# Optimization experiments

Measured on AMD Instinct MI355X. Metric: run time of the kernel, lower is better.

The kernel has to match this reference:

```python
import jax, jax.numpy as jnp
import numpy as np

N = 100000
E = 1600000
IN_FEATS = 512
HIDDEN = 128
NUM_CLASSES = 2


def setup_inputs() -> dict:
    key = jax.random.key(0)
    k1, k2, k3, k4, k5, k6, k7 = jax.random.split(key, 7)
    inputs = jax.random.normal(k1, (N, IN_FEATS), dtype=jnp.float32)
    src = jax.random.randint(k2, (E,), 0, N, dtype=jnp.int64)
    dst = jax.random.randint(k3, (E,), 0, N, dtype=jnp.int64)
    # Glorot-style init like DGL GraphConv
    s1 = (6.0 / (IN_FEATS + HIDDEN)) ** 0.5
    s2 = (6.0 / (HIDDEN + NUM_CLASSES)) ** 0.5
    W1 = jax.random.uniform(k4, (IN_FEATS, HIDDEN), jnp.float32, -s1, s1)
    b1 = jnp.zeros((HIDDEN,), jnp.float32)
    W2 = jax.random.uniform(k5, (HIDDEN, NUM_CLASSES), jnp.float32, -s2, s2)
    b2 = jnp.zeros((NUM_CLASSES,), jnp.float32)
    return {"inputs": inputs, "W1": W1, "b1": b1, "W2": W2, "b2": b2,
            "src": src, "dst": dst}


def _graph_conv(x, W, b, src, dst, norm_src, norm_dst):
    # DGL GraphConv, norm='both': D_dst^{-1/2} A D_src^{-1/2} X W + b
    xw = x @ W                                   # [N, out] dense GEMM first (in >= out)
    m = (xw * norm_src[:, None])[src]            # gather messages [E, out]
    agg = jax.ops.segment_sum(m, dst, num_segments=N)  # scatter-add [N, out]
    return agg * norm_dst[:, None] + b


def reference(inputs, W1, b1, W2, b2, src, dst):
    ones = jnp.ones((src.shape[0],), jnp.float32)
    out_deg = jax.ops.segment_sum(ones, src, num_segments=N)
    in_deg = jax.ops.segment_sum(ones, dst, num_segments=N)
    norm_src = jax.lax.rsqrt(jnp.maximum(out_deg, 1.0))
    norm_dst = jax.lax.rsqrt(jnp.maximum(in_deg, 1.0))

    h = _graph_conv(inputs, W1, b1, src, dst, norm_src, norm_dst)
    h = jax.nn.relu(h)
    # dropout is identity at inference (training=False)
    h = _graph_conv(h, W2, b2, src, dst, norm_src, norm_dst)
    return jax.nn.softmax(h, axis=1)
```

## Files before the change

### kernel.cpp

```cpp
#include <hip/hip_runtime.h>
#include <math.h>

#define N_NODES 100000
#define N_EDGES 1600000
#define IN_F    512
#define HID     128

#define SH      8
#define NPB     256
#define BINS    ((N_NODES + NPB - 1) / NPB)
#define CBLK    256
#define EPB     ((N_EDGES + CBLK - 1) / CBLK)

typedef __attribute__((ext_vector_type(8))) _Float16 half8;
typedef __attribute__((ext_vector_type(2))) _Float16 half2v;
typedef __attribute__((ext_vector_type(4))) float float4v;

__device__ __forceinline__ unsigned int f16_to_e4m3bits(float xs) {
    _Float16 h = (_Float16)xs;
    unsigned short b = __builtin_bit_cast(unsigned short, h);
    unsigned int mag = (unsigned int)(b & 0x7fffu);
    mag = (mag + 0x3fu + ((mag >> 7) & 1u)) >> 7;
    if (mag > 0x7eu) mag = 0x7eu;
    return (((unsigned int)b >> 8) & 0x80u) | mag;
}

__global__ __launch_bounds__(256) void prep_kernel(const float* __restrict__ W1,
                                                   _Float16* __restrict__ W1T,
                                                   int* __restrict__ sdeg) {
    int i = blockIdx.x * 256 + threadIdx.x;
    if (i < IN_F * HID) {
        int k = i >> 7, c = i & 127;
        W1T[(size_t)c * IN_F + k] = (_Float16)W1[i];
    }
    if (i < N_NODES) sdeg[i] = 0;
}

__global__ __launch_bounds__(256) void hist_kernel(const int* __restrict__ src,
                                                   const int* __restrict__ dst,
                                                   int* __restrict__ dbh,
                                                   int* __restrict__ sdeg) {
    __shared__ int hd[BINS];
    const int t = threadIdx.x, blk = blockIdx.x;
    for (int i = t; i < BINS; i += 256) hd[i] = 0;
    __syncthreads();
    const int e0 = blk * EPB, e1 = min(N_EDGES, e0 + EPB);
    for (int e = e0 + t; e < e1; e += 256) {
        atomicAdd(&hd[dst[e] >> SH], 1);
        atomicAdd(&sdeg[src[e]], 1);
    }
    __syncthreads();
    for (int i = t; i < BINS; i += 256)
        dbh[i * CBLK + blk] = hd[i];
}

__global__ __launch_bounds__(256) void binscan_kernel(int* __restrict__ dbh,
                                                      int* __restrict__ dtot) {
    __shared__ int sh[256];
    const int b = blockIdx.x, t = threadIdx.x;
    int* arr = dbh + (size_t)b * CBLK;
    int v = arr[t];
    sh[t] = v; __syncthreads();
#pragma unroll
    for (int d = 1; d < 256; d <<= 1) {
        int u = (t >= d) ? sh[t - d] : 0;
        __syncthreads();
        sh[t] += u;
        __syncthreads();
    }
    arr[t] = sh[t] - v;
    if (t == 255) dtot[b] = sh[255];
}

__global__ __launch_bounds__(512) void binbase_kernel(const int* __restrict__ dtot,
                                                      int* __restrict__ dbase,
                                                      int* __restrict__ offs) {
    __shared__ int sh[512];
    const int t = threadIdx.x;
    int v = (t < BINS) ? dtot[t] : 0;
    sh[t] = v; __syncthreads();
#pragma unroll
    for (int d = 1; d < 512; d <<= 1) {
        int u = (t >= d) ? sh[t - d] : 0;
        __syncthreads();
        sh[t] += u;
        __syncthreads();
    }
    if (t < BINS) dbase[t] = sh[t] - v;
    if (t == BINS - 1) { dbase[BINS] = sh[t]; offs[N_NODES] = sh[t]; }
}

__global__ __launch_bounds__(256) void scatter_bins_kernel(const int* __restrict__ src,
                                                           const int* __restrict__ dst,
                                                           const int* __restrict__ dbh,
                                                           const int* __restrict__ dbase,
                                                           unsigned int* __restrict__ es) {
    __shared__ int dcur[BINS];
    const int t = threadIdx.x, blk = blockIdx.x;
    for (int i = t; i < BINS; i += 256)
        dcur[i] = dbase[i] + dbh[i * CBLK + blk];
    __syncthreads();
    const int e0 = blk * EPB, e1 = min(N_EDGES, e0 + EPB);
    for (int e = e0 + t; e < e1; e += 256) {
        int d = dst[e], s = src[e];
        int p = atomicAdd(&dcur[d >> SH], 1);
        es[p] = ((unsigned int)(d & (NPB - 1)) << 24) | (unsigned int)s;
    }
}

__global__ __launch_bounds__(256) void finalize_kernel(const unsigned int* __restrict__ es,
                                                       const int* __restrict__ sdeg,
                                                       const int* __restrict__ dbase,
                                                       int* __restrict__ csr, int* __restrict__ offs,
                                                       float* __restrict__ norm_dst,
                                                       float* __restrict__ norm_src) {
    __shared__ int cnt[NPB], pos[NPB];
    const int t = threadIdx.x, b = blockIdx.x;
    const int start = dbase[b], end = dbase[b + 1];
    cnt[t] = 0; __syncthreads();
    for (int k = start + t; k < end; k += 256)
        atomicAdd(&cnt[es[k] >> 24], 1);
    __syncthreads();
    const int c = cnt[t];
    pos[t] = c; __syncthreads();
#pragma unroll
    for (int d = 1; d < 256; d <<= 1) {
        int u = (t >= d) ? pos[t - d] : 0;
        __syncthreads();
        pos[t] += u;
        __syncthreads();
    }
    const int excl = pos[t] - c;
    const int node = (b << SH) + t;
    if (node < N_NODES) {
        offs[node] = start + excl;
        norm_dst[node] = rsqrtf(fmaxf((float)c, 1.0f));
        norm_src[node] = rsqrtf(fmaxf((float)sdeg[node], 1.0f));
    }
    cnt[t] = start + excl;
    __syncthreads();
    for (int k = start + t; k < end; k += 256) {
        unsigned int v = es[k];
        int p = atomicAdd(&cnt[v >> 24], 1);
        csr[p] = (int)(v & 0x00FFFFFFu);
    }
}

__global__ __launch_bounds__(256) void gemm1_mfma_kernel(const float* __restrict__ X,
                                                         const _Float16* __restrict__ W1T,
                                                         const float* __restrict__ norm_src,
                                                         unsigned int* __restrict__ xw8) {
    const int t    = threadIdx.x;
    const int wave = t >> 6;
    const int lane = t & 63;
    const int quad = lane >> 4;
    const int l16  = lane & 15;
    const int wrow = blockIdx.x * 64 + wave * 16;
    const int arow = wrow + l16;
    const int crow = (arow < N_NODES) ? arow : 0;
    const float*    xa = X   + (size_t)crow * IN_F + quad * 8;
    const _Float16* wb = W1T + (size_t)l16  * IN_F + quad * 8;

    float4v acc[8];
#pragma unroll
    for (int c = 0; c < 8; c++) acc[c] = (float4v)0.f;

    float4 A[2][2];
    half8  B[8];
    {
        const float4* p0 = reinterpret_cast<const float4*>(xa);
        A[0][0] = p0[0]; A[0][1] = p0[1];
        const float4* p1 = reinterpret_cast<const float4*>(xa + 32);
        A[1][0] = p1[0]; A[1][1] = p1[1];
#pragma unroll
        for (int ct = 0; ct < 8; ct++)
            B[ct] = *reinterpret_cast<const half8*>(wb + (size_t)(ct * 16) * IN_F);
    }

#pragma unroll
    for (int it = 0; it < 16; ++it) {
        const int cur = it & 1;
        half8 fa;
        fa[0] = (_Float16)A[cur][0].x; fa[1] = (_Float16)A[cur][0].y;
        fa[2] = (_Float16)A[cur][0].z; fa[3] = (_Float16)A[cur][0].w;
        fa[4] = (_Float16)A[cur][1].x; fa[5] = (_Float16)A[cur][1].y;
        fa[6] = (_Float16)A[cur][1].z; fa[7] = (_Float16)A[cur][1].w;
        if (it + 2 < 16) {
            const float4* p = reinterpret_cast<const float4*>(xa + (it + 2) * 32);
            A[cur][0] = p[0]; A[cur][1] = p[1];
        }
        half8 Bc[8];
#pragma unroll
        for (int ct = 0; ct < 8; ct++) Bc[ct] = B[ct];
        if (it + 1 < 16) {
#pragma unroll
            for (int ct = 0; ct < 8; ct++)
                B[ct] = *reinterpret_cast<const half8*>(
                    wb + (size_t)(ct * 16) * IN_F + (it + 1) * 32);
        }
#pragma unroll
        for (int ct = 0; ct < 8; ct++)
            acc[ct] = __builtin_amdgcn_mfma_f32_16x16x32_f16(fa, Bc[ct], acc[ct], 0, 0, 0);
    }

    const int grow = wrow + quad * 4;
#pragma unroll
    for (int i = 0; i < 4; i++) {
        const int g = grow + i;
        if (g < N_NODES) {
            const float ss = norm_src[g] * 0.00390625f;
            unsigned int by[8];
#pragma unroll
            for (int ct = 0; ct < 8; ct++) {
                float xs = acc[ct][i] * ss;
                xs = fminf(fmaxf(xs, -1.75f), 1.75f);
                by[ct] = f16_to_e4m3bits(xs);
            }
            unsigned int w0 = by[0] | (by[1] << 8) | (by[2] << 16) | (by[3] << 24);
            unsigned int w1 = by[4] | (by[5] << 8) | (by[6] << 16) | (by[7] << 24);
            *reinterpret_cast<uint2*>(&xw8[(size_t)g * 32 + l16 * 2]) = make_uint2(w0, w1);
        }
    }
}

__global__ __launch_bounds__(256) void gather1_kernel(
        const int* __restrict__ csr, const int* __restrict__ offs,
        const unsigned int* __restrict__ xw8, const float* __restrict__ norm_dst,
        const float* __restrict__ norm_src, const float* __restrict__ b1,
        const float* __restrict__ W2, float* __restrict__ hw2) {
    const int gw   = (blockIdx.x * blockDim.x + threadIdx.x) >> 6;
    const int lane = threadIdx.x & 63;
    const int sub  = lane >> 4;
    const int l16  = lane & 15;
    const int n    = gw * 4 + sub;
    if (n >= N_NODES) return;
    const int off = offs[n], end = offs[n + 1];
    const uint2* xp = reinterpret_cast<const uint2*>(xw8);

    half2v accA = (half2v)0, accB = (half2v)0, accC = (half2v)0, accD = (half2v)0;

#define DECADD(u, aE, aO)                                                          \
    {                                                                              \
        unsigned int _u = (u);                                                     \
        unsigned int _e = ((_u & 0x00800080u) << 8) | ((_u & 0x007f007fu) << 7);   \
        unsigned int _s = _u >> 8;                                                 \
        unsigned int _o = ((_s & 0x00800080u) << 8) | ((_s & 0x007f007fu) << 7);   \
        aE += __builtin_bit_cast(half2v, _e);                                      \
        aO += __builtin_bit_cast(half2v, _o);                                      \
    }
#define ACC8(u2) { DECADD((u2).x, accA, accB) DECADD((u2).y, accC, accD) }

    int k = off;
    for (; k + 8 <= end; k += 8) {
        int s0 = csr[k], s1 = csr[k + 1], s2 = csr[k + 2], s3 = csr[k + 3];
        int s4 = csr[k + 4], s5 = csr[k + 5], s6 = csr[k + 6], s7 = csr[k + 7];
        uint2 u0 = xp[(size_t)s0 * 16 + l16];
        uint2 u1 = xp[(size_t)s1 * 16 + l16];
        uint2 u2 = xp[(size_t)s2 * 16 + l16];
        uint2 u3 = xp[(size_t)s3 * 16 + l16];
        uint2 u4 = xp[(size_t)s4 * 16 + l16];
        uint2 u5 = xp[(size_t)s5 * 16 + l16];
        uint2 u6 = xp[(size_t)s6 * 16 + l16];
        uint2 u7 = xp[(size_t)s7 * 16 + l16];
        ACC8(u0) ACC8(u1) ACC8(u2) ACC8(u3) ACC8(u4) ACC8(u5) ACC8(u6) ACC8(u7)
    }
    for (; k + 4 <= end; k += 4) {
        int s0 = csr[k], s1 = csr[k + 1], s2 = csr[k + 2], s3 = csr[k + 3];
        uint2 u0 = xp[(size_t)s0 * 16 + l16];
        uint2 u1 = xp[(size_t)s1 * 16 + l16];
        uint2 u2 = xp[(size_t)s2 * 16 + l16];
        uint2 u3 = xp[(size_t)s3 * 16 + l16];
        ACC8(u0) ACC8(u1) ACC8(u2) ACC8(u3)
    }
    for (; k < end; ++k) {
        uint2 u = xp[(size_t)csr[k] * 16 + l16];
        ACC8(u)
    }
#undef ACC8
#undef DECADD

    float a[8];
    a[0] = (float)accA[0]; a[2] = (float)accA[1];
    a[1] = (float)accB[0]; a[3] = (float)accB[1];
    a[4] = (float)accC[0]; a[6] = (float)accC[1];
    a[5] = (float)accD[0]; a[7] = (float)accD[1];

    const float nd = norm_dst[n] * 256.0f;
    float p0 = 0.f, p1 = 0.f;
#pragma unroll
    for (int ct = 0; ct < 8; ct++) {
        const int col = ct * 16 + l16;
        float h = fmaxf(a[ct] * nd + b1[col], 0.f);
        float2 w2v = reinterpret_cast<const float2*>(W2)[col];
        p0 += h * w2v.x;
        p1 += h * w2v.y;
    }
#pragma unroll
    for (int d = 1; d < 16; d <<= 1) {
        p0 += __shfl_xor(p0, d);
        p1 += __shfl_xor(p1, d);
    }
    if (l16 == 0) {
        float ns = norm_src[n];
        reinterpret_cast<float2*>(hw2)[n] = make_float2(p0 * ns, p1 * ns);
    }
}

__global__ void gather2_softmax_kernel(
        const int* __restrict__ csr, const int* __restrict__ offs,
        const float* __restrict__ hw2, const float* __restrict__ norm_dst,
        const float* __restrict__ b2, float* __restrict__ out) {
    const int w    = (blockIdx.x * blockDim.x + threadIdx.x) >> 6;
    const int lane = threadIdx.x & 63;
    const int sub  = lane >> 4, k0 = lane & 15;
    const int n = w * 4 + sub;
    if (n >= N_NODES) return;
    const int off = offs[n], end = offs[n + 1];

    float a0 = 0.f, a1 = 0.f;
    for (int k = off + k0; k < end; k += 16) {
        int s = csr[k];
        float2 v = reinterpret_cast<const float2*>(hw2)[s];
        a0 += v.x; a1 += v.y;
    }
#pragma unroll
    for (int d = 1; d < 16; d <<= 1) {
        a0 += __shfl_xor(a0, d);
        a1 += __shfl_xor(a1, d);
    }
    if (k0 == 0) {
        float nd = norm_dst[n];
        float z0 = a0 * nd + b2[0];
        float z1 = a1 * nd + b2[1];
        float m = fmaxf(z0, z1);
        float e0 = expf(z0 - m), e1 = expf(z1 - m);
        float inv = 1.f / (e0 + e1);
        reinterpret_cast<float2*>(out)[n] = make_float2(e0 * inv, e1 * inv);
    }
}

extern "C" void kernel_launch(void* const* d_in, const int* in_sizes, int n_in,
                              void* d_out, int out_size, void* d_ws, size_t ws_size,
                              hipStream_t stream) {
    const float* X   = (const float*)d_in[0];
    const float* W1  = (const float*)d_in[1];
    const float* b1  = (const float*)d_in[2];
    const float* W2  = (const float*)d_in[3];
    const float* b2  = (const float*)d_in[4];
    const int*   src = (const int*)d_in[5];
    const int*   dst = (const int*)d_in[6];
    float* out = (float*)d_out;

    const size_t N = N_NODES;
    char* ws = (char*)d_ws;
    auto alloc = [&](size_t bytes) -> char* {
        char* p = ws;
        ws += (bytes + 15) & ~(size_t)15;
        return p;
    };
    int*          dbh      = (int*)alloc((size_t)BINS * CBLK * 4);
    int*          dtot     = (int*)alloc(BINS * 4);
    int*          dbase    = (int*)alloc((BINS + 1) * 4);
    int*          sdeg     = (int*)alloc(N * 4);
    unsigned int* es       = (unsigned int*)alloc((size_t)N_EDGES * 4);
    int*          csr      = (int*)alloc((size_t)N_EDGES * 4);
    int*          offs     = (int*)alloc((N + 1) * 4);
    float*        norm_src = (float*)alloc(N * 4);
    float*        norm_dst = (float*)alloc(N * 4);
    float*        hw2      = (float*)alloc(N * 2 * 4);
    _Float16*     W1T      = (_Float16*)alloc((size_t)IN_F * HID * 2);
    unsigned int* xw8      = (unsigned int*)alloc(N * (size_t)HID);

    prep_kernel<<<(N_NODES + 255) / 256, 256, 0, stream>>>(W1, W1T, sdeg);
    hist_kernel<<<CBLK, 256, 0, stream>>>(src, dst, dbh, sdeg);
    binscan_kernel<<<BINS, 256, 0, stream>>>(dbh, dtot);
    binbase_kernel<<<1, 512, 0, stream>>>(dtot, dbase, offs);
    scatter_bins_kernel<<<CBLK, 256, 0, stream>>>(src, dst, dbh, dbase, es);
    finalize_kernel<<<BINS, 256, 0, stream>>>(es, sdeg, dbase,
                                              csr, offs, norm_dst, norm_src);
    gemm1_mfma_kernel<<<(N_NODES + 63) / 64, 256, 0, stream>>>(X, W1T, norm_src, xw8);
    gather1_kernel<<<(((N_NODES + 3) / 4) * 64 + 255) / 256, 256, 0, stream>>>(
        csr, offs, xw8, norm_dst, norm_src, b1, W2, hw2);
    gather2_softmax_kernel<<<(((int)N + 3) / 4 * 64 + 255) / 256, 256, 0, stream>>>(
        csr, offs, hw2, norm_dst, b2, out);
}
```

Baseline: 557.6 us.

## Stage GEMM1 A tile through double-buffered shared memory with coalesced loads

The first-layer GEMM now loads X rows cooperatively with coalesced float4 reads, converts them to fp16 and stores them into a padded double-buffered LDS tile. Each wave then reads its MFMA A fragment from LDS instead of strided per-lane global loads. This targets poor coalescing of the per-lane global X reads, at the cost of a __syncthreads per K step and a loop that is no longer fully unrolled, which may reduce latency hiding.

Result: faster. 514.8 us (-7.7%).

```diff
diff --git a/kernel.cpp b/kernel.cpp
--- a/kernel.cpp
+++ b/kernel.cpp
@@ -146,64 +146,87 @@
     }
 }
 
+#define APAD 40
 __global__ __launch_bounds__(256) void gemm1_mfma_kernel(const float* __restrict__ X,
                                                          const _Float16* __restrict__ W1T,
                                                          const float* __restrict__ norm_src,
                                                          unsigned int* __restrict__ xw8) {
+    __shared__ _Float16 As[2][64 * APAD];
+
     const int t    = threadIdx.x;
     const int wave = t >> 6;
     const int lane = t & 63;
+    const int m0   = blockIdx.x * 64;
     const int quad = lane >> 4;
     const int l16  = lane & 15;
-    const int wrow = blockIdx.x * 64 + wave * 16;
-    const int arow = wrow + l16;
-    const int crow = (arow < N_NODES) ? arow : 0;
-    const float*    xa = X   + (size_t)crow * IN_F + quad * 8;
-    const _Float16* wb = W1T + (size_t)l16  * IN_F + quad * 8;
 
     float4v acc[8];
 #pragma unroll
     for (int c = 0; c < 8; c++) acc[c] = (float4v)0.f;
 
-    float4 A[2][2];
-    half8  B[8];
+    const int srow = t >> 2;
+    const int scol = (t & 3) * 8;
+    const int sgrow = m0 + srow;
+    const bool svalid = sgrow < N_NODES;
+    const float* xbase = X + (size_t)sgrow * IN_F + scol;
+
+    float4 va[2];
+    va[0] = va[1] = make_float4(0.f, 0.f, 0.f, 0.f);
+    if (svalid) {
+        const float4* xp = reinterpret_cast<const float4*>(xbase);
+        va[0] = xp[0]; va[1] = xp[1];
+    }
+    half8 bfrag[8];
+#pragma unroll
+    for (int ct = 0; ct < 8; ct++)
+        bfrag[ct] = *reinterpret_cast<const half8*>(&W1T[(size_t)(ct * 16 + l16) * IN_F + quad * 8]);
+
     {
-        const float4* p0 = reinterpret_cast<const float4*>(xa);
-        A[0][0] = p0[0]; A[0][1] = p0[1];
-        const float4* p1 = reinterpret_cast<const float4*>(xa + 32);
-        A[1][0] = p1[0]; A[1][1] = p1[1];
+        half8 h;
+        h[0]=(_Float16)va[0].x; h[1]=(_Float16)va[0].y; h[2]=(_Float16)va[0].z; h[3]=(_Float16)va[0].w;
+        h[4]=(_Float16)va[1].x; h[5]=(_Float16)va[1].y; h[6]=(_Float16)va[1].z; h[7]=(_Float16)va[1].w;
+        *reinterpret_cast<half8*>(&As[0][srow * APAD + scol]) = h;
+    }
+
+    int cur = 0;
+    for (int it = 0; it < IN_F / 32; it++) {
+        const int ktn = (it + 1) * 32;
+        const bool more = ktn < IN_F;
+        __syncthreads();
+
+        float4 vb[2];
+        half8 bnext[8];
+        if (more) {
+            if (svalid) {
+                const float4* xp = reinterpret_cast<const float4*>(xbase + ktn);
+                vb[0] = xp[0]; vb[1] = xp[1];
+            } else {
+                vb[0] = vb[1] = make_float4(0.f, 0.f, 0.f, 0.f);
+            }
+#pragma unroll
+            for (int ct = 0; ct < 8; ct++)
+                bnext[ct] = *reinterpret_cast<const half8*>(
+                    &W1T[(size_t)(ct * 16 + l16) * IN_F + ktn + quad * 8]);
+        }
+
+        half8 afrag = *reinterpret_cast<const half8*>(
+            &As[cur][(wave * 16 + l16) * APAD + quad * 8]);
 #pragma unroll
         for (int ct = 0; ct < 8; ct++)
-            B[ct] = *reinterpret_cast<const half8*>(wb + (size_t)(ct * 16) * IN_F);
-    }
-
-#pragma unroll
-    for (int it = 0; it < 16; ++it) {
-        const int cur = it & 1;
-        half8 fa;
-        fa[0] = (_Float16)A[cur][0].x; fa[1] = (_Float16)A[cur][0].y;
-        fa[2] = (_Float16)A[cur][0].z; fa[3] = (_Float16)A[cur][0].w;
-        fa[4] = (_Float16)A[cur][1].x; fa[5] = (_Float16)A[cur][1].y;
-        fa[6] = (_Float16)A[cur][1].z; fa[7] = (_Float16)A[cur][1].w;
-        if (it + 2 < 16) {
-            const float4* p = reinterpret_cast<const float4*>(xa + (it + 2) * 32);
-            A[cur][0] = p[0]; A[cur][1] = p[1];
+            acc[ct] = __builtin_amdgcn_mfma_f32_16x16x32_f16(afrag, bfrag[ct], acc[ct], 0, 0, 0);
+
+        if (more) {
+            half8 h;
+            h[0]=(_Float16)vb[0].x; h[1]=(_Float16)vb[0].y; h[2]=(_Float16)vb[0].z; h[3]=(_Float16)vb[0].w;
+            h[4]=(_Float16)vb[1].x; h[5]=(_Float16)vb[1].y; h[6]=(_Float16)vb[1].z; h[7]=(_Float16)vb[1].w;
+            *reinterpret_cast<half8*>(&As[cur ^ 1][srow * APAD + scol]) = h;
+#pragma unroll
+            for (int ct = 0; ct < 8; ct++) bfrag[ct] = bnext[ct];
         }
-        half8 Bc[8];
-#pragma unroll
-        for (int ct = 0; ct < 8; ct++) Bc[ct] = B[ct];
-        if (it + 1 < 16) {
-#pragma unroll
-            for (int ct = 0; ct < 8; ct++)
-                B[ct] = *reinterpret_cast<const half8*>(
-                    wb + (size_t)(ct * 16) * IN_F + (it + 1) * 32);
-        }
-#pragma unroll
-        for (int ct = 0; ct < 8; ct++)
-            acc[ct] = __builtin_amdgcn_mfma_f32_16x16x32_f16(fa, Bc[ct], acc[ct], 0, 0, 0);
-    }
-
-    const int grow = wrow + quad * 4;
+        cur ^= 1;
+    }
+
+    const int grow = m0 + wave * 16 + quad * 4;
 #pragma unroll
     for (int i = 0; i < 4; i++) {
         const int g = grow + i;
```
